# Kernel tuning notes

Measured on AMD Instinct MI355X. Metric: run time of the kernel, lower is better.

The kernel has to match this reference:

```python
import jax, jax.numpy as jnp
import numpy as np

B, S, H = 1, 1024, 1024
E = 1024          # expert_dim
NEXP = 16         # num_experts
TOPK = 2
ALPHA = 1.702
LIMIT = 7.0


def setup_inputs() -> dict:
    key = jax.random.key(0)
    ks = jax.random.split(key, 8)
    hidden_states = jax.random.normal(ks[0], (B, S, H), dtype=jnp.float32)
    # router (gate): Linear(H, NEXP) with bias
    Wg = jax.random.normal(ks[1], (NEXP, H), dtype=jnp.float32) / np.sqrt(H)
    bg = jax.random.normal(ks[2], (NEXP,), dtype=jnp.float32) * 0.01
    # per-expert gate_up_proj: Linear(H, 2E) -> store as [NEXP, H, 2E]
    Wgu = jax.random.normal(ks[3], (NEXP, H, 2 * E), dtype=jnp.float32) / np.sqrt(H)
    bgu = jax.random.normal(ks[4], (NEXP, 2 * E), dtype=jnp.float32) * 0.01
    # per-expert down_proj: Linear(E, H) -> store as [NEXP, E, H]
    Wd = jax.random.normal(ks[5], (NEXP, E, H), dtype=jnp.float32) / np.sqrt(E)
    bd = jax.random.normal(ks[6], (NEXP, H), dtype=jnp.float32) * 0.01
    return {"hidden_states": hidden_states, "Wg": Wg, "bg": bg,
            "Wgu": Wgu, "bgu": bgu, "Wd": Wd, "bd": bd}


def _moe_forward(x, Wg, bg, Wgu, bgu, Wd, bd):
    b, s, h = x.shape
    xt = x.reshape(-1, h)                                   # [T, H]
    # router
    logits = xt @ Wg.T + bg                                 # [T, NEXP]
    # gpt_oss routing: topk over raw logits, softmax over selected
    top_vals, top_idx = jax.lax.top_k(logits, TOPK)         # [T, K]
    rw = jax.nn.softmax(top_vals.astype(jnp.float32), axis=-1).astype(xt.dtype)
    # combine weight per (token, expert): zero for unselected experts
    onehot = jax.nn.one_hot(top_idx, NEXP, dtype=xt.dtype)  # [T, K, NEXP]
    cw = jnp.einsum("tk,tke->te", rw, onehot)               # [T, NEXP]
    # dense expert compute (reference math identical to gather/scatter version)
    gu = jnp.einsum("th,ehf->tef", xt, Wgu) + bgu[None]     # [T, NEXP, 2E]
    gate = gu[..., ::2]
    up = gu[..., 1::2]
    gate = jnp.minimum(gate, LIMIT)
    up = jnp.clip(up, -LIMIT, LIMIT)
    glu = gate * jax.nn.sigmoid(gate * ALPHA)
    gated = (up + 1.0) * glu                                # [T, NEXP, E]
    out_e = jnp.einsum("tef,efh->teh", gated, Wd) + bd[None]  # [T, NEXP, H]
    out = jnp.einsum("teh,te->th", out_e, cw)               # [T, H]
    return out.reshape(b, s, h)


def reference(hidden_states, Wg, bg, Wgu, bgu, Wd, bd):
    return _moe_forward(hidden_states, Wg, bg, Wgu, bgu, Wd, bd)
```

## Files before the change

kernel.cpp:

```cpp
#include <hip/hip_runtime.h>
#include <hip/hip_bf16.h>

#define NT 1024
#define HD 1024
#define ED 1024
#define F2D 2048
#define NEXPERT 16
#define GROWS 2304
#define ALPHA_C 1.702f
#define LIMIT_C 7.0f

typedef float f32x4 __attribute__((ext_vector_type(4)));
typedef float fv4 __attribute__((ext_vector_type(4)));
typedef short short8 __attribute__((ext_vector_type(8)));
typedef unsigned int u32x4 __attribute__((ext_vector_type(4)));

__device__ __forceinline__ unsigned short f2bf(float x) {
  union { float f; unsigned int u; } v; v.f = x;
  unsigned int r = v.u + 0x7FFFu + ((v.u >> 16) & 1u);
  return (unsigned short)(r >> 16);
}
__device__ __forceinline__ unsigned int pk2(float lo, float hi) {
  return (unsigned int)f2bf(lo) | ((unsigned int)f2bf(hi) << 16);
}
__device__ __forceinline__ fv4 ldnt4(const float* p) {
  return __builtin_nontemporal_load((const fv4*)p);
}
__device__ __forceinline__ void async16(const void* g, void* l) {
  __builtin_amdgcn_global_load_lds((const __attribute__((address_space(1))) void*)g,
                                   (__attribute__((address_space(3))) void*)l, 16, 0, 0);
}

#define BT_TRANSPOSE_STORE(DST)                                                         \
  {                                                                                     \
    unsigned int w0p = pk2(b0[0], b1[0]);                                               \
    unsigned int w1p = pk2(b0[1], b1[1]);                                               \
    unsigned int w2p = pk2(b0[2], b1[2]);                                               \
    unsigned int w3p = pk2(b0[3], b1[3]);                                               \
    unsigned int X0 = sub == 0 ? w0p : sub == 1 ? w1p : sub == 2 ? w2p : w3p;           \
    unsigned int X1 = sub == 0 ? w1p : sub == 1 ? w0p : sub == 2 ? w3p : w2p;           \
    unsigned int X2 = sub == 0 ? w2p : sub == 1 ? w3p : sub == 2 ? w0p : w1p;           \
    unsigned int X3 = sub == 0 ? w3p : sub == 1 ? w2p : sub == 2 ? w1p : w0p;           \
    unsigned int r0 = X0;                                                               \
    unsigned int r1 = (unsigned int)__builtin_amdgcn_update_dpp((int)X1, (int)X1, 0xB1, 0xF, 0xF, 0); \
    unsigned int r2 = (unsigned int)__builtin_amdgcn_update_dpp((int)X2, (int)X2, 0x4E, 0xF, 0xF, 0); \
    unsigned int r3 = (unsigned int)__builtin_amdgcn_update_dpp((int)X3, (int)X3, 0x1B, 0xF, 0xF, 0); \
    u32x4 tt;                                                                           \
    tt[0] = sub == 0 ? r0 : sub == 1 ? r1 : sub == 2 ? r2 : r3;                         \
    tt[1] = sub == 0 ? r1 : sub == 1 ? r0 : sub == 2 ? r3 : r2;                         \
    tt[2] = sub == 0 ? r2 : sub == 1 ? r3 : sub == 2 ? r0 : r1;                         \
    tt[3] = sub == 0 ? r3 : sub == 1 ? r2 : sub == 2 ? r1 : r0;                         \
    *(u32x4*)(DST) = tt;                                                                \
  }

__global__ __launch_bounds__(256) void k_router(const float* __restrict__ x,
                                                const float* __restrict__ Wg,
                                                const float* __restrict__ bg,
                                                const float* __restrict__ bd,
                                                int* __restrict__ e01,
                                                float* __restrict__ w0f,
                                                float* __restrict__ w1f,
                                                unsigned short* __restrict__ Xbf,
                                                float* __restrict__ out) {
  const int t = blockIdx.x;
  const int tid = threadIdx.x;
  const int w = tid >> 6;
  const int l = tid & 63;
  const float4* x4 = (const float4*)(x + (size_t)t * HD);
  {
    float4 v = x4[tid];
    unsigned int* dst = (unsigned int*)(Xbf + (size_t)t * HD + tid * 4);
    dst[0] = pk2(v.x, v.y); dst[1] = pk2(v.z, v.w);
  }
  const int e = l & 15, qq = l >> 4;
  const float4* wg4 = (const float4*)(Wg + (size_t)e * HD);
  float s = 0.f;
#pragma unroll 4
  for (int j = 0; j < 16; ++j) {
    const int idx = w * 64 + qq + 4 * j;
    float4 a = x4[idx], b = wg4[idx];
    s += a.x * b.x + a.y * b.y + a.z * b.z + a.w * b.w;
  }
  s += __shfl_xor(s, 16);
  s += __shfl_xor(s, 32);
  __shared__ float slog[4][16];
  if (l < 16) slog[w][e] = s;
  __syncthreads();
  float v0 = -1e30f, v1 = -1e30f; int i0 = 0, i1 = 0;
  for (int k2 = 0; k2 < 16; ++k2) {
    float lv = slog[0][k2] + slog[1][k2] + slog[2][k2] + slog[3][k2] + bg[k2];
    if (lv > v0) { v1 = v0; i1 = i0; v0 = lv; i0 = k2; }
    else if (lv > v1) { v1 = lv; i1 = k2; }
  }
  const float w0 = 1.f / (1.f + __expf(v1 - v0));
  const float w1 = 1.f - w0;
  if (tid == 0) {
    e01[t] = i0 | (i1 << 8);
    w0f[t] = w0;
    w1f[t] = w1;
  }
  const float4* bd0 = (const float4*)(bd + (size_t)i0 * HD);
  const float4* bd1 = (const float4*)(bd + (size_t)i1 * HD);
  float4 a = bd0[tid], b = bd1[tid];
  float4 r;
  r.x = w0 * a.x + w1 * b.x;
  r.y = w0 * a.y + w1 * b.y;
  r.z = w0 * a.z + w1 * b.z;
  r.w = w0 * a.w + w1 * b.w;
  ((float4*)(out + (size_t)t * HD))[tid] = r;
}

__global__ __launch_bounds__(1024) void k_scan(const int* __restrict__ e01,
                                               const float* __restrict__ w0f,
                                               const float* __restrict__ w1f,
                                               int* __restrict__ cnt,
                                               int* __restrict__ off,
                                               int* __restrict__ gtok,
                                               float* __restrict__ gwt) {
  __shared__ int scnt[NEXPERT];
  __shared__ int soff[NEXPERT];
  __shared__ int scur[NEXPERT];
  const int t = threadIdx.x;
  if (t < NEXPERT) { scnt[t] = 0; scur[t] = 0; }
  __syncthreads();
  const int p = e01[t];
  const int e0 = p & 255, e1 = p >> 8;
  atomicAdd(&scnt[e0], 1);
  atomicAdd(&scnt[e1], 1);
  __syncthreads();
  if (t == 0) {
    int a = 0;
    for (int e = 0; e < NEXPERT; ++e) { soff[e] = a; off[e] = a; cnt[e] = scnt[e]; a += scnt[e]; }
  }
  __syncthreads();
  int s0 = atomicAdd(&scur[e0], 1);
  gtok[soff[e0] + s0] = t; gwt[soff[e0] + s0] = w0f[t];
  int s1 = atomicAdd(&scur[e1], 1);
  gtok[soff[e1] + s1] = t; gwt[soff[e1] + s1] = w1f[t];
}

__global__ __launch_bounds__(256) void k_gemm1(const unsigned short* __restrict__ Xbf,
                                               const float* __restrict__ Wgu,
                                               const float* __restrict__ bgu,
                                               const int* __restrict__ cnt,
                                               const int* __restrict__ off,
                                               const int* __restrict__ gtok,
                                               unsigned short* __restrict__ Gact) {
  const int e = blockIdx.z;
  const int Ne = cnt[e];
  const int mtile = blockIdx.y;
  if (mtile * 256 >= Ne) return;
  const int ntile = blockIdx.x;
  const int tid = threadIdx.x;
  const int lane = tid & 63;
  const int wv = tid >> 6;
  const int q = lane >> 4;
  const int fr = lane & 15;
  const int xq = q ^ ((fr >> 1) & 3);
  const int base = off[e] + mtile * 256;

  __shared__ unsigned short AldsL[3 * 8192];
  __shared__ unsigned int BldsL[3 * 1024];

  const int arow = tid >> 2;
  const int cs = (tid & 3) ^ ((arow >> 1) & 3);
  const unsigned short* agp[4];
#pragma unroll
  for (int j = 0; j < 4; ++j) {
    const int r = arow + j * 64;
    const int ags = base + (((mtile * 256 + r) < Ne) ? r : 0);
    agp[j] = Xbf + (size_t)gtok[ags] * HD + cs * 8;
  }
  const int aofs = tid * 8;

  const int sub = tid & 3;
  const int quad = tid >> 2;
  const int colgrp = quad & 15;
  const int kblock = quad >> 4;
  const float* Wb = Wgu + (size_t)e * HD * F2D + (size_t)(2 * (kblock * 4 + sub)) * F2D + ntile * 64 + colgrp * 4;
  const int bcol = colgrp * 4 + sub;
  const int bofs = bcol * 16 + (kblock ^ ((bcol >> 1) & 3)) * 4;

  f32x4 acc[4][4] = {};
  fv4 b0A, b1A, b0B, b1B;

  b0A = ldnt4(Wb);
  b1A = ldnt4(Wb + F2D);
#pragma unroll
  for (int j = 0; j < 4; ++j)
    async16(agp[j], AldsL + aofs + j * 2048);
  b0B = ldnt4(Wb + (size_t)32 * F2D);
  b1B = ldnt4(Wb + (size_t)33 * F2D);
#pragma unroll
  for (int j = 0; j < 4; ++j)
    async16(agp[j] + 32, AldsL + 8192 + aofs + j * 2048);
  asm volatile("s_waitcnt vmcnt(6)" ::: "memory");
  __builtin_amdgcn_sched_barrier(0);
  { fv4 b0 = b0A, b1 = b1A; BT_TRANSPOSE_STORE(BldsL + bofs) }
  asm volatile("s_waitcnt lgkmcnt(0)" ::: "memory");
  __builtin_amdgcn_s_barrier();
  __builtin_amdgcn_sched_barrier(0);

  int cur = 0, nx1 = 1, nx2 = 2;
  for (int ks = 0; ks < 32; ++ks) {
    short8 af[4], bfr[4];
    const unsigned short* Ab = AldsL + cur * 8192;
    const unsigned int* Bb = BldsL + cur * 1024;
#pragma unroll
    for (int mi = 0; mi < 4; ++mi)
      af[mi] = *(const short8*)(Ab + (wv * 64 + mi * 16 + fr) * 32 + xq * 8);
#pragma unroll
    for (int ni = 0; ni < 4; ++ni)
      bfr[ni] = *(const short8*)(Bb + (ni * 16 + fr) * 16 + xq * 4);
    if (ks < 30) {
      const float* bp = Wb + (size_t)(ks + 2) * 32 * F2D;
      if ((ks & 1) == 0) { b0A = ldnt4(bp); b1A = ldnt4(bp + F2D); }
      else               { b0B = ldnt4(bp); b1B = ldnt4(bp + F2D); }
      unsigned short* Adst = AldsL + nx2 * 8192 + aofs;
#pragma unroll
      for (int j = 0; j < 4; ++j)
        async16(agp[j] + (ks + 2) * 32, Adst + j * 2048);
    }
#pragma unroll
    for (int mi = 0; mi < 4; ++mi)
#pragma unroll
      for (int ni = 0; ni < 4; ++ni)
        acc[mi][ni] = __builtin_amdgcn_mfma_f32_16x16x32_bf16(af[mi], bfr[ni], acc[mi][ni], 0, 0, 0);
    if (ks < 30) {
      asm volatile("s_waitcnt vmcnt(6)" ::: "memory");
      __builtin_amdgcn_sched_barrier(0);
    } else if (ks == 30) {
      asm volatile("s_waitcnt vmcnt(0)" ::: "memory");
      __builtin_amdgcn_sched_barrier(0);
    }
    if (ks < 31) {
      fv4 b0 = (ks & 1) ? b0A : b0B;
      fv4 b1 = (ks & 1) ? b1A : b1B;
      BT_TRANSPOSE_STORE(BldsL + nx1 * 1024 + bofs)
      asm volatile("s_waitcnt lgkmcnt(0)" ::: "memory");
      __builtin_amdgcn_s_barrier();
      __builtin_amdgcn_sched_barrier(0);
    }
    const int tmp = cur; cur = nx1; nx1 = nx2; nx2 = tmp;
  }

  const float* bguE = bgu + (size_t)e * F2D + ntile * 64;
#pragma unroll
  for (int mi = 0; mi < 4; ++mi) {
#pragma unroll
    for (int ni = 0; ni < 4; ++ni) {
      const int coll = ni * 16 + fr;
      const float bias = bguE[coll];
#pragma unroll
      for (int r = 0; r < 4; ++r) {
        const int srow = wv * 64 + mi * 16 + q * 4 + r;
        float v = acc[mi][ni][r] + bias;
        float pv = __shfl_xor(v, 1);
        float gate = (lane & 1) ? pv : v;
        float up   = (lane & 1) ? v : pv;
        gate = fminf(gate, LIMIT_C);
        up = fminf(fmaxf(up, -LIMIT_C), LIMIT_C);
        float glu = gate / (1.f + __expf(-ALPHA_C * gate));
        float val = (up + 1.f) * glu;
        if (!(lane & 1) && (mtile * 256 + srow) < Ne)
          Gact[(size_t)(base + srow) * ED + ((ntile * 64 + coll) >> 1)] = f2bf(val);
      }
    }
  }
}

#define BSTG2T 20
__global__ __launch_bounds__(512, 2) void k_gemm2(const unsigned short* __restrict__ Gact,
                                                  const float* __restrict__ Wd,
                                                  const int* __restrict__ cnt,
                                                  const int* __restrict__ off,
                                                  const int* __restrict__ gtok,
                                                  const float* __restrict__ gwt,
                                                  float* __restrict__ out) {
  const int e = blockIdx.z;
  const int Ne = cnt[e];
  const int mtile = blockIdx.y;
  if (mtile * 256 >= Ne) return;
  const int ntile = blockIdx.x;
  const int tid = threadIdx.x;
  const int lane = tid & 63;
  const int wv = tid >> 6;
  const int q = lane >> 4;
  const int fr = lane & 15;
  const int base = off[e] + mtile * 256;

  __shared__ unsigned short Alds[2][256 * 32];
  __shared__ unsigned int Blds[2][64 * BSTG2T];

  const int ar0 = wv * 32 + (lane >> 2);
  const unsigned short* agp0 = Gact + (size_t)(base + ar0) * ED + (lane & 3) * 8;
  const unsigned short* agp1 = agp0 + (size_t)16 * ED;
  const int aofs = wv * 1024;

  const int sub = lane & 3;
  const float* Wb = Wd + (size_t)e * ED * HD + (size_t)(2 * (wv * 4 + sub)) * HD + ntile * 64 + (lane >> 2) * 4;
  const int bofs = lane * BSTG2T + wv * 4;

  f32x4 acc[2][4] = {};
  fv4 b0, b1;

  if (tid < 256) {
    b0 = ldnt4(Wb);
    b1 = ldnt4(Wb + HD);
  }
  async16(agp0, Alds[0] + aofs);
  async16(agp1, Alds[0] + aofs + 512);
  if (tid < 256) BT_TRANSPOSE_STORE(Blds[0] + bofs)
  __syncthreads();

  for (int ks = 0; ks < 32; ++ks) {
    const int cur = ks & 1, nxt = cur ^ 1;
    const bool more = (ks + 1) < 32;
    if (more) {
      if (tid < 256) {
        const float* bp = Wb + (size_t)(ks + 1) * 32 * HD;
        b0 = ldnt4(bp);
        b1 = ldnt4(bp + HD);
      }
      async16(agp0 + (ks + 1) * 32, Alds[nxt] + aofs);
      async16(agp1 + (ks + 1) * 32, Alds[nxt] + aofs + 512);
    }
    short8 af[2], bfr[4];
#pragma unroll
    for (int mi = 0; mi < 2; ++mi)
      af[mi] = *(const short8*)(Alds[cur] + (wv * 32 + mi * 16 + fr) * 32 + q * 8);
#pragma unroll
    for (int ni = 0; ni < 4; ++ni)
      bfr[ni] = *(const short8*)(Blds[cur] + (ni * 16 + fr) * BSTG2T + q * 4);
#pragma unroll
    for (int mi = 0; mi < 2; ++mi)
#pragma unroll
      for (int ni = 0; ni < 4; ++ni)
        acc[mi][ni] = __builtin_amdgcn_mfma_f32_16x16x32_bf16(af[mi], bfr[ni], acc[mi][ni], 0, 0, 0);
    if (more && tid < 256) BT_TRANSPOSE_STORE(Blds[nxt] + bofs)
    __syncthreads();
  }

#pragma unroll
  for (int mi = 0; mi < 2; ++mi) {
#pragma unroll
    for (int r = 0; r < 4; ++r) {
      const int srow = wv * 32 + mi * 16 + q * 4 + r;
      if ((mtile * 256 + srow) < Ne) {
        const int gsl = base + srow;
        const int tok = gtok[gsl];
        const float wt = gwt[gsl];
        float* op = out + (size_t)tok * HD + ntile * 64;
#pragma unroll
        for (int ni = 0; ni < 4; ++ni) {
          const int col = ni * 16 + fr;
          atomicAdd(op + col, wt * acc[mi][ni][r]);
        }
      }
    }
  }
}

extern "C" void kernel_launch(void* const* d_in, const int* in_sizes, int n_in,
                              void* d_out, int out_size, void* d_ws, size_t ws_size,
                              hipStream_t stream) {
  const float* x   = (const float*)d_in[0];
  const float* Wg  = (const float*)d_in[1];
  const float* bg  = (const float*)d_in[2];
  const float* Wgu = (const float*)d_in[3];
  const float* bgu = (const float*)d_in[4];
  const float* Wd  = (const float*)d_in[5];
  const float* bd  = (const float*)d_in[6];
  float* out = (float*)d_out;

  int* cnt = (int*)d_ws;
  int* off = cnt + 16;
  int* e01 = off + 16;
  float* w0f = (float*)(e01 + NT);
  float* w1f = w0f + NT;
  int* gtok = (int*)(w1f + NT);
  float* gwt = (float*)(gtok + GROWS);
  unsigned short* Xbf = (unsigned short*)(gwt + GROWS);
  unsigned short* Gact = Xbf + (size_t)NT * HD;

  k_router<<<NT, 256, 0, stream>>>(x, Wg, bg, bd, e01, w0f, w1f, Xbf, out);
  k_scan<<<1, NT, 0, stream>>>(e01, w0f, w1f, cnt, off, gtok, gwt);
  k_gemm1<<<dim3(32, 2, NEXPERT), 256, 0, stream>>>(Xbf, Wgu, bgu, cnt, off, gtok, Gact);
  k_gemm2<<<dim3(16, 2, NEXPERT), 512, 0, stream>>>(Gact, Wd, cnt, off, gtok, gwt, out);
}
```

Baseline: 323.7 us.

## Shrink gemm1 M-tile to 128 rows with 128-thread blocks for finer expert tiling

```diff
diff --git a/kernel.cpp b/kernel.cpp
--- a/kernel.cpp
+++ b/kernel.cpp
@@ -139,7 +139,7 @@
   gtok[soff[e1] + s1] = t; gwt[soff[e1] + s1] = w1f[t];
 }
 
-__global__ __launch_bounds__(256) void k_gemm1(const unsigned short* __restrict__ Xbf,
+__global__ __launch_bounds__(128) void k_gemm1(const unsigned short* __restrict__ Xbf,
                                                const float* __restrict__ Wgu,
                                                const float* __restrict__ bgu,
                                                const int* __restrict__ cnt,
@@ -149,7 +149,7 @@
   const int e = blockIdx.z;
   const int Ne = cnt[e];
   const int mtile = blockIdx.y;
-  if (mtile * 256 >= Ne) return;
+  if (mtile * 128 >= Ne) return;
   const int ntile = blockIdx.x;
   const int tid = threadIdx.x;
   const int lane = tid & 63;
@@ -157,9 +157,9 @@
   const int q = lane >> 4;
   const int fr = lane & 15;
   const int xq = q ^ ((fr >> 1) & 3);
-  const int base = off[e] + mtile * 256;
-
-  __shared__ unsigned short AldsL[3 * 8192];
+  const int base = off[e] + mtile * 128;
+
+  __shared__ unsigned short AldsL[3 * 4096];
   __shared__ unsigned int BldsL[3 * 1024];
 
   const int arow = tid >> 2;
@@ -167,8 +167,8 @@
   const unsigned short* agp[4];
 #pragma unroll
   for (int j = 0; j < 4; ++j) {
-    const int r = arow + j * 64;
-    const int ags = base + (((mtile * 256 + r) < Ne) ? r : 0);
+    const int r = arow + j * 32;
+    const int ags = base + (((mtile * 128 + r) < Ne) ? r : 0);
     agp[j] = Xbf + (size_t)gtok[ags] * HD + cs * 8;
   }
   const int aofs = tid * 8;
@@ -176,27 +176,32 @@
   const int sub = tid & 3;
   const int quad = tid >> 2;
   const int colgrp = quad & 15;
-  const int kblock = quad >> 4;
-  const float* Wb = Wgu + (size_t)e * HD * F2D + (size_t)(2 * (kblock * 4 + sub)) * F2D + ntile * 64 + colgrp * 4;
+  const int kbh = quad >> 4;
+  const int kb0 = kbh, kb1 = kbh + 2;
   const int bcol = colgrp * 4 + sub;
-  const int bofs = bcol * 16 + (kblock ^ ((bcol >> 1) & 3)) * 4;
+  const float* WbBase = Wgu + (size_t)e * HD * F2D + ntile * 64 + colgrp * 4;
+  const float* Wb0 = WbBase + (size_t)(2 * (kb0 * 4 + sub)) * F2D;
+  const float* Wb1 = WbBase + (size_t)(2 * (kb1 * 4 + sub)) * F2D;
+  const int bofs0 = bcol * 16 + (kb0 ^ ((bcol >> 1) & 3)) * 4;
+  const int bofs1 = bcol * 16 + (kb1 ^ ((bcol >> 1) & 3)) * 4;
 
   f32x4 acc[4][4] = {};
-  fv4 b0A, b1A, b0B, b1B;
-
-  b0A = ldnt4(Wb);
-  b1A = ldnt4(Wb + F2D);
+  fv4 b0A, b1A, c0A, c1A, b0B, b1B, c0B, c1B;
+
+  b0A = ldnt4(Wb0); b1A = ldnt4(Wb0 + F2D);
+  c0A = ldnt4(Wb1); c1A = ldnt4(Wb1 + F2D);
 #pragma unroll
   for (int j = 0; j < 4; ++j)
-    async16(agp[j], AldsL + aofs + j * 2048);
-  b0B = ldnt4(Wb + (size_t)32 * F2D);
-  b1B = ldnt4(Wb + (size_t)33 * F2D);
+    async16(agp[j], AldsL + aofs + j * 1024);
+  b0B = ldnt4(Wb0 + (size_t)32 * F2D); b1B = ldnt4(Wb0 + (size_t)33 * F2D);
+  c0B = ldnt4(Wb1 + (size_t)32 * F2D); c1B = ldnt4(Wb1 + (size_t)33 * F2D);
 #pragma unroll
   for (int j = 0; j < 4; ++j)
-    async16(agp[j] + 32, AldsL + 8192 + aofs + j * 2048);
-  asm volatile("s_waitcnt vmcnt(6)" ::: "memory");
+    async16(agp[j] + 32, AldsL + 4096 + aofs + j * 1024);
+  asm volatile("s_waitcnt vmcnt(8)" ::: "memory");
   __builtin_amdgcn_sched_barrier(0);
-  { fv4 b0 = b0A, b1 = b1A; BT_TRANSPOSE_STORE(BldsL + bofs) }
+  { fv4 b0 = b0A, b1 = b1A; BT_TRANSPOSE_STORE(BldsL + bofs0) }
+  { fv4 b0 = c0A, b1 = c1A; BT_TRANSPOSE_STORE(BldsL + bofs1) }
   asm volatile("s_waitcnt lgkmcnt(0)" ::: "memory");
   __builtin_amdgcn_s_barrier();
   __builtin_amdgcn_sched_barrier(0);
@@ -204,7 +209,7 @@
   int cur = 0, nx1 = 1, nx2 = 2;
   for (int ks = 0; ks < 32; ++ks) {
     short8 af[4], bfr[4];
-    const unsigned short* Ab = AldsL + cur * 8192;
+    const unsigned short* Ab = AldsL + cur * 4096;
     const unsigned int* Bb = BldsL + cur * 1024;
 #pragma unroll
     for (int mi = 0; mi < 4; ++mi)
@@ -213,13 +218,18 @@
     for (int ni = 0; ni < 4; ++ni)
       bfr[ni] = *(const short8*)(Bb + (ni * 16 + fr) * 16 + xq * 4);
     if (ks < 30) {
-      const float* bp = Wb + (size_t)(ks + 2) * 32 * F2D;
-      if ((ks & 1) == 0) { b0A = ldnt4(bp); b1A = ldnt4(bp + F2D); }
-      else               { b0B = ldnt4(bp); b1B = ldnt4(bp + F2D); }
-      unsigned short* Adst = AldsL + nx2 * 8192 + aofs;
+      const size_t ko = (size_t)(ks + 2) * 32 * F2D;
+      if ((ks & 1) == 0) {
+        b0A = ldnt4(Wb0 + ko); b1A = ldnt4(Wb0 + ko + F2D);
+        c0A = ldnt4(Wb1 + ko); c1A = ldnt4(Wb1 + ko + F2D);
+      } else {
+        b0B = ldnt4(Wb0 + ko); b1B = ldnt4(Wb0 + ko + F2D);
+        c0B = ldnt4(Wb1 + ko); c1B = ldnt4(Wb1 + ko + F2D);
+      }
+      unsigned short* Adst = AldsL + nx2 * 4096 + aofs;
 #pragma unroll
       for (int j = 0; j < 4; ++j)
-        async16(agp[j] + (ks + 2) * 32, Adst + j * 2048);
+        async16(agp[j] + (ks + 2) * 32, Adst + j * 1024);
     }
 #pragma unroll
     for (int mi = 0; mi < 4; ++mi)
@@ -227,16 +237,20 @@
       for (int ni = 0; ni < 4; ++ni)
         acc[mi][ni] = __builtin_amdgcn_mfma_f32_16x16x32_bf16(af[mi], bfr[ni], acc[mi][ni], 0, 0, 0);
     if (ks < 30) {
-      asm volatile("s_waitcnt vmcnt(6)" ::: "memory");
+      asm volatile("s_waitcnt vmcnt(8)" ::: "memory");
       __builtin_amdgcn_sched_barrier(0);
     } else if (ks == 30) {
       asm volatile("s_waitcnt vmcnt(0)" ::: "memory");
       __builtin_amdgcn_sched_barrier(0);
     }
     if (ks < 31) {
-      fv4 b0 = (ks & 1) ? b0A : b0B;
-      fv4 b1 = (ks & 1) ? b1A : b1B;
-      BT_TRANSPOSE_STORE(BldsL + nx1 * 1024 + bofs)
+      if (ks & 1) {
+        { fv4 b0 = b0A, b1 = b1A; BT_TRANSPOSE_STORE(BldsL + nx1 * 1024 + bofs0) }
+        { fv4 b0 = c0A, b1 = c1A; BT_TRANSPOSE_STORE(BldsL + nx1 * 1024 + bofs1) }
+      } else {
+        { fv4 b0 = b0B, b1 = b1B; BT_TRANSPOSE_STORE(BldsL + nx1 * 1024 + bofs0) }
+        { fv4 b0 = c0B, b1 = c1B; BT_TRANSPOSE_STORE(BldsL + nx1 * 1024 + bofs1) }
+      }
       asm volatile("s_waitcnt lgkmcnt(0)" ::: "memory");
       __builtin_amdgcn_s_barrier();
       __builtin_amdgcn_sched_barrier(0);
@@ -262,7 +276,7 @@
         up = fminf(fmaxf(up, -LIMIT_C), LIMIT_C);
         float glu = gate / (1.f + __expf(-ALPHA_C * gate));
         float val = (up + 1.f) * glu;
-        if (!(lane & 1) && (mtile * 256 + srow) < Ne)
+        if (!(lane & 1) && (mtile * 128 + srow) < Ne)
           Gact[(size_t)(base + srow) * ED + ((ntile * 64 + coll) >> 1)] = f2bf(val);
       }
     }
@@ -385,6 +399,6 @@
 
   k_router<<<NT, 256, 0, stream>>>(x, Wg, bg, bd, e01, w0f, w1f, Xbf, out);
   k_scan<<<1, NT, 0, stream>>>(e01, w0f, w1f, cnt, off, gtok, gwt);
-  k_gemm1<<<dim3(32, 2, NEXPERT), 256, 0, stream>>>(Xbf, Wgu, bgu, cnt, off, gtok, Gact);
+  k_gemm1<<<dim3(32, 4, NEXPERT), 128, 0, stream>>>(Xbf, Wgu, bgu, cnt, off, gtok, Gact);
   k_gemm2<<<dim3(16, 2, NEXPERT), 512, 0, stream>>>(Gact, Wd, cnt, off, gtok, gwt, out);
 }
```

Result: slower. 342.0 us (+5.7%).
